# Kernel optimization log

Measured on AMD Instinct MI355X. Metric: run time of the kernel, lower is better.

## Reference

```python
import jax, jax.numpy as jnp
import numpy as np

EPS = 1e-5
MAX_NORM = 1.0 - EPS
K = 16
ALPHA = 0.1
TAU = 0.1  # softmax temperature in forward


def project(x):
    # enforce ||x|| < 1 on the Poincare ball
    n = jnp.clip(jnp.linalg.norm(x, axis=-1, keepdims=True), EPS, None)
    return x / jnp.maximum(n / MAX_NORM, 1.0)


def mobius_add(u, v):
    c = 1.0
    dot_uv = jnp.sum(u * v, axis=-1, keepdims=True)
    nu = jnp.clip(jnp.sum(u * u, axis=-1, keepdims=True), 0.0, MAX_NORM ** 2)
    nv = jnp.clip(jnp.sum(v * v, axis=-1, keepdims=True), 0.0, MAX_NORM ** 2)
    num = (1 + 2 * c * dot_uv + c * nv) * u + (1 - c * nu) * v
    den = 1 + 2 * c * dot_uv + c * c * nu * nv
    return project(num / jnp.clip(den, EPS, None))


def exp_map(x, v):
    # sqrt_c = 1
    vn = jnp.clip(jnp.linalg.norm(v, axis=-1, keepdims=True), EPS, None)
    second = jnp.tanh(vn / 2.0) * v / vn
    return mobius_add(x, second)


def poincare_cdist(q, mem):
    # q: [B, M], mem: [N, M] -> [B, N] geodesic distances (c=1)
    qn = jnp.clip(jnp.sum(q * q, axis=-1), 0.0, MAX_NORM ** 2)          # [B]
    mn = jnp.clip(jnp.sum(mem * mem, axis=-1), 0.0, MAX_NORM ** 2)      # [N]
    # ||q - m||^2 expanded via gram matrix (same math as diff-based form)
    dist_sq = jnp.clip(jnp.sum(q * q, axis=-1)[:, None] + jnp.sum(mem * mem, axis=-1)[None, :]
                       - 2.0 * q @ mem.T, 0.0, None)                     # [B, N]
    den = (1.0 - qn)[:, None] * (1.0 - mn)[None, :]
    x = 2.0 * dist_sq / jnp.clip(den, EPS, None)
    return jnp.arccosh(1.0 + x)


def layernorm(x, g, b):
    mu = jnp.mean(x, axis=-1, keepdims=True)
    var = jnp.mean((x - mu) ** 2, axis=-1, keepdims=True)
    return (x - mu) / jnp.sqrt(var + 1e-5) * g + b


def setup_inputs() -> dict:
    key = jax.random.key(0)
    ks = jax.random.split(key, 10)
    B, S, H, M, N = 32, 2048, 1024, 128, 500000
    hidden_states = jax.random.normal(ks[0], (B, S, H), dtype=jnp.float32)
    W1 = jax.random.normal(ks[1], (H, M), dtype=jnp.float32) * 0.02
    b1 = jnp.zeros((M,), dtype=jnp.float32)
    ln_g = jnp.ones((M,), dtype=jnp.float32)
    ln_b = jnp.zeros((M,), dtype=jnp.float32)
    W2 = jax.random.normal(ks[2], (M, M), dtype=jnp.float32) * 0.02
    b2 = jnp.zeros((M,), dtype=jnp.float32)
    q_origin = jnp.zeros((1, M), dtype=jnp.float32)
    memory = project(jax.random.normal(ks[3], (N, M), dtype=jnp.float32) * 0.3)
    Wp = jax.random.normal(ks[4], (M, H), dtype=jnp.float32) * 0.02
    bp = jnp.zeros((H,), dtype=jnp.float32)
    return {"hidden_states": hidden_states, "W1": W1, "b1": b1, "ln_g": ln_g,
            "ln_b": ln_b, "W2": W2, "b2": b2, "q_origin": q_origin,
            "memory": memory, "Wp": Wp, "bp": bp}


def reference(hidden_states, W1, b1, ln_g, ln_b, W2, b2, q_origin, memory, Wp, bp):
    B, S, H = hidden_states.shape
    # query network on mean-pooled hidden states
    pooled = jnp.mean(hidden_states, axis=1)                  # [B, H]
    h = pooled @ W1 + b1                                      # [B, M]
    h = jax.nn.gelu(layernorm(h, ln_g, ln_b), approximate=False)
    tangent = h @ W2 + b2                                     # [B, M]
    origin = project(jnp.broadcast_to(q_origin, (B, q_origin.shape[-1])))
    query = exp_map(origin, tangent)                          # [B, M] on ball
    # geodesic kNN over the memory bank
    dists = poincare_cdist(query, memory)                     # [B, N]
    neg_top, idx = jax.lax.top_k(-dists, K)                   # smallest K
    top_d = -neg_top                                          # [B, K]
    neighbors = memory[idx]                                   # [B, K, M]
    w = jax.nn.softmax(-top_d / TAU, axis=-1)                 # [B, K]
    retrieved = jnp.einsum('bk,bkm->bm', w, neighbors)        # [B, M]
    force = retrieved @ Wp + bp                               # [B, H]
    return hidden_states + ALPHA * force[:, None, :]
```

## Files before the change

### kernel.cpp

```cpp
#include <hip/hip_runtime.h>
#include <float.h>
#include <math.h>

#define B_ 32
#define S_ 2048
#define H_ 1024
#define M_ 128
#define N_ 500000
#define KK 16
#define KK2 32
#define ALPHA_ 0.1f
#define TAU_ 0.1f
#define EPS_ 1e-5f
#define MAX_NORM_ 0.99999f
#define MAXN2_ (MAX_NORM_ * MAX_NORM_)
#define SC_ 64
#define RPB_ 512
#define NBLK_ ((N_ + RPB_ - 1) / RPB_)
#define WIN_ 2048
#define NWIN_ ((N_ + WIN_ - 1) / WIN_)
#define NPAD_ (NWIN_ * WIN_)

typedef __attribute__((ext_vector_type(8))) short short8;
typedef __attribute__((ext_vector_type(4))) float f32x4;

__device__ __forceinline__ unsigned short to_bf16(float x) {
    unsigned u = __float_as_uint(x);
    return (unsigned short)((u + 0x7FFFu + ((u >> 16) & 1u)) >> 16);
}

__global__ __launch_bounds__(256) void k1_pool(const float* __restrict__ hid,
                                               float* __restrict__ pp) {
    int bid = blockIdx.x;
    int b = bid >> 6, sc = bid & 63;
    const float4* h4 = (const float4*)hid;
    float4 acc = {0.f, 0.f, 0.f, 0.f};
    int s0 = sc * (S_ / SC_);
    for (int s = 0; s < S_ / SC_; ++s) {
        float4 v = h4[((size_t)(b * S_ + s0 + s) << 8) + threadIdx.x];
        acc.x += v.x; acc.y += v.y; acc.z += v.z; acc.w += v.w;
    }
    ((float4*)pp)[(size_t)(b * SC_ + sc) * 256 + threadIdx.x] = acc;
}

__device__ __forceinline__ float block_reduce_sum_128(float v, volatile float* red, int tid) {
    red[tid] = v;
    __syncthreads();
    if (tid < 64) red[tid] += red[tid + 64];
    __syncthreads();
    if (tid < 64) {
        float x = red[tid];
        #pragma unroll
        for (int off = 32; off >= 1; off >>= 1) x += __shfl_down(x, off);
        if (tid == 0) red[0] = x;
    }
    __syncthreads();
    float r = red[0];
    __syncthreads();
    return r;
}

__global__ void k2_query(const float* __restrict__ pp, const float* __restrict__ W1,
                         const float* __restrict__ b1, const float* __restrict__ ln_g,
                         const float* __restrict__ ln_b, const float* __restrict__ W2,
                         const float* __restrict__ b2, const float* __restrict__ qorig,
                         float* __restrict__ query, float* __restrict__ qstats) {
    __shared__ float pooled[H_];
    __shared__ float red[128];
    __shared__ float hv[M_];
    int b = blockIdx.x, tid = threadIdx.x;
    #pragma unroll
    for (int j = 0; j < H_ / 128; ++j) {
        int h = tid + j * 128;
        float s = 0.f;
        for (int sc = 0; sc < SC_; ++sc) s += pp[(size_t)(b * SC_ + sc) * H_ + h];
        pooled[h] = s * (1.0f / (float)S_);
    }
    __syncthreads();
    int m = tid;
    float x = b1[m];
    for (int k = 0; k < H_; ++k) x = fmaf(pooled[k], W1[k * M_ + m], x);
    float mu = block_reduce_sum_128(x, red, tid) * (1.0f / (float)M_);
    float dmu = x - mu;
    float var = block_reduce_sum_128(dmu * dmu, red, tid) * (1.0f / (float)M_);
    float xh = dmu * rsqrtf(var + 1e-5f) * ln_g[m] + ln_b[m];
    float g = 0.5f * xh * (1.0f + erff(xh * 0.70710678f));
    hv[m] = g;
    __syncthreads();
    float t = b2[m];
    for (int k = 0; k < M_; ++k) t = fmaf(hv[k], W2[k * M_ + m], t);
    float o = qorig[m];
    float on2 = block_reduce_sum_128(o * o, red, tid);
    float on = fmaxf(sqrtf(on2), EPS_);
    float osc = 1.0f / fmaxf(on / MAX_NORM_, 1.0f);
    float u = o * osc;
    float vn2 = block_reduce_sum_128(t * t, red, tid);
    float vn = fmaxf(sqrtf(vn2), EPS_);
    float sec = tanhf(vn * 0.5f) * t / vn;
    float dot_uv = block_reduce_sum_128(u * sec, red, tid);
    float nu = fminf(fmaxf(block_reduce_sum_128(u * u, red, tid), 0.f), MAXN2_);
    float nv = fminf(fmaxf(block_reduce_sum_128(sec * sec, red, tid), 0.f), MAXN2_);
    float num = (1.0f + 2.0f * dot_uv + nv) * u + (1.0f - nu) * sec;
    float den = 1.0f + 2.0f * dot_uv + nu * nv;
    float r = num / fmaxf(den, EPS_);
    float rn2 = block_reduce_sum_128(r * r, red, tid);
    float rn = fmaxf(sqrtf(rn2), EPS_);
    float rsc = 1.0f / fmaxf(rn / MAX_NORM_, 1.0f);
    float q = r * rsc;
    query[b * M_ + m] = q;
    float qq = block_reduce_sum_128(q * q, red, tid);
    if (tid == 0) {
        qstats[b * 2 + 0] = qq;
        float qn = fminf(fmaxf(qq, 0.f), MAXN2_);
        qstats[b * 2 + 1] = 1.0f - qn;
    }
}

__global__ __launch_bounds__(256, 3) void k3_scores(const float* __restrict__ mem,
                                                    const float* __restrict__ query,
                                                    const float* __restrict__ qstats,
                                                    unsigned short* __restrict__ keyplane) {
    __shared__ unsigned short key_lds[B_][264];
    __shared__ float mm_lds[256];
    __shared__ float qq_s[B_], omq_s[B_];
    int tid = threadIdx.x, bid = blockIdx.x;
    int wave = tid >> 6, lane = tid & 63;
    int l15 = lane & 15, lk = lane >> 4;

    if (tid < B_) { qq_s[tid] = qstats[tid * 2]; omq_s[tid] = qstats[tid * 2 + 1]; }

    short8 bfrag[2][4];
    #pragma unroll
    for (int bg = 0; bg < 2; ++bg) {
        #pragma unroll
        for (int kt = 0; kt < 4; ++kt) {
            int batch = bg * 16 + l15;
            const float4* qp = (const float4*)(query + batch * M_ + kt * 32 + lk * 8);
            float4 lo = qp[0], hi = qp[1];
            short8 f;
            f[0] = (short)to_bf16(lo.x); f[1] = (short)to_bf16(lo.y);
            f[2] = (short)to_bf16(lo.z); f[3] = (short)to_bf16(lo.w);
            f[4] = (short)to_bf16(hi.x); f[5] = (short)to_bf16(hi.y);
            f[6] = (short)to_bf16(hi.z); f[7] = (short)to_bf16(hi.w);
            bfrag[bg][kt] = f;
        }
    }

    #pragma unroll 1
    for (int p = 0; p < 2; ++p) {
        int passbase = bid * RPB_ + p * 256;
        f32x4 acc[4][2];
        #pragma unroll
        for (int rg = 0; rg < 4; ++rg)
            #pragma unroll
            for (int bg = 0; bg < 2; ++bg)
                acc[rg][bg] = (f32x4){0.f, 0.f, 0.f, 0.f};
        float mmp[4] = {0.f, 0.f, 0.f, 0.f};

        #pragma unroll
        for (int rg = 0; rg < 4; ++rg) {
            int r = passbase + wave * 64 + rg * 16 + l15;
            const float4* mp = (const float4*)(mem + (size_t)((r < N_) ? r : 0) * M_);
            #pragma unroll
            for (int kt = 0; kt < 4; ++kt) {
                float4 lo = mp[kt * 8 + lk * 2];
                float4 hi = mp[kt * 8 + lk * 2 + 1];
                mmp[rg] = fmaf(lo.x, lo.x, fmaf(lo.y, lo.y, fmaf(lo.z, lo.z, fmaf(lo.w, lo.w, mmp[rg]))));
                mmp[rg] = fmaf(hi.x, hi.x, fmaf(hi.y, hi.y, fmaf(hi.z, hi.z, fmaf(hi.w, hi.w, mmp[rg]))));
                short8 af;
                af[0] = (short)to_bf16(lo.x); af[1] = (short)to_bf16(lo.y);
                af[2] = (short)to_bf16(lo.z); af[3] = (short)to_bf16(lo.w);
                af[4] = (short)to_bf16(hi.x); af[5] = (short)to_bf16(hi.y);
                af[6] = (short)to_bf16(hi.z); af[7] = (short)to_bf16(hi.w);
                acc[rg][0] = __builtin_amdgcn_mfma_f32_16x16x32_bf16(af, bfrag[0][kt], acc[rg][0], 0, 0, 0);
                acc[rg][1] = __builtin_amdgcn_mfma_f32_16x16x32_bf16(af, bfrag[1][kt], acc[rg][1], 0, 0, 0);
            }
        }
        #pragma unroll
        for (int rg = 0; rg < 4; ++rg) {
            float v = mmp[rg] + __shfl_xor(mmp[rg], 16);
            v += __shfl_xor(v, 32);
            if (lane < 16) mm_lds[wave * 64 + rg * 16 + l15] = v;
        }
        __syncthreads();

        #pragma unroll
        for (int rg = 0; rg < 4; ++rg) {
            #pragma unroll
            for (int bg = 0; bg < 2; ++bg) {
                #pragma unroll
                for (int reg = 0; reg < 4; ++reg) {
                    int row_local = wave * 64 + rg * 16 + lk * 4 + reg;
                    int batch = bg * 16 + l15;
                    float dot = acc[rg][bg][reg];
                    float mmv = mm_lds[row_local];
                    float mn = fminf(mmv, MAXN2_);
                    float dsq = fmaxf(qq_s[batch] + mmv - 2.0f * dot, 0.f);
                    float t = dsq / fmaxf(omq_s[batch] * (1.0f - mn), EPS_);
                    key_lds[batch][row_local] = to_bf16(t);
                }
            }
        }
        __syncthreads();

        {
            int batch = tid >> 3, chunk = tid & 7;
            int rbase = passbase + chunk * 32;
            unsigned short* dstp = keyplane + (size_t)batch * NPAD_ + rbase;
            #pragma unroll
            for (int i = 0; i < 4; ++i) {
                int gr = rbase + i * 8;
                uint4 v = *(const uint4*)&key_lds[batch][chunk * 32 + i * 8];
                if (gr + 8 <= N_) {
                    *(uint4*)(dstp + i * 8) = v;
                } else {
                    for (int t = 0; t < 8; ++t)
                        if (gr + t < N_) dstp[i * 8 + t] = key_lds[batch][chunk * 32 + i * 8 + t];
                }
            }
        }
        __syncthreads();
    }
}

__global__ __launch_bounds__(256, 4) void k4_sel(const unsigned short* __restrict__ keyplane,
                                                 unsigned* __restrict__ cand_key) {
    int win = blockIdx.x >> 2, quad = blockIdx.x & 3;
    int wave = threadIdx.x >> 6, lane = threadIdx.x & 63;
    int base = win * WIN_;
    #pragma unroll 1
    for (int j = 0; j < 2; ++j) {
        int b = quad * 8 + wave * 2 + j;
        const uint4* kp = (const uint4*)(keyplane + (size_t)b * NPAD_ + base);
        unsigned keys[32];
        #pragma unroll
        for (int i = 0; i < 4; ++i) {
            uint4 v = kp[lane + i * 64];
            int rl0 = (lane + i * 64) * 8;
            int pos = base + rl0;
            unsigned s[8];
            s[0] = v.x & 0xFFFFu; s[1] = v.x >> 16;
            s[2] = v.y & 0xFFFFu; s[3] = v.y >> 16;
            s[4] = v.z & 0xFFFFu; s[5] = v.z >> 16;
            s[6] = v.w & 0xFFFFu; s[7] = v.w >> 16;
            #pragma unroll
            for (int t = 0; t < 8; ++t)
                keys[i * 8 + t] = (pos + t < N_) ? ((s[t] << 11) | (unsigned)(rl0 + t))
                                                 : 0xFFFFFFFFu;
        }
        for (int k = 0; k < KK; ++k) {
            unsigned m = keys[0];
            #pragma unroll
            for (int i = 1; i < 32; ++i) m = min(m, keys[i]);
            #pragma unroll
            for (int off = 32; off >= 1; off >>= 1)
                m = min(m, (unsigned)__shfl_xor((int)m, off));
            if (lane == 0) cand_key[((size_t)win * B_ + b) * KK + k] = m;
            #pragma unroll
            for (int i = 0; i < 32; ++i)
                if (keys[i] == m) keys[i] = 0xFFFFFFFFu;
        }
    }
}

__global__ void k45_retrieve(const unsigned* __restrict__ cand_key,
                             const float* __restrict__ mem, const float* __restrict__ query,
                             const float* __restrict__ qstats,
                             const float* __restrict__ Wp, const float* __restrict__ bp,
                             float* __restrict__ force) {
    __shared__ unsigned tv[256 * KK];
    __shared__ int ti[256 * KK];
    __shared__ unsigned mv[64 * KK];
    __shared__ int mi[64 * KK];
    __shared__ int top32_s[KK2];
    __shared__ float q_s[M_];
    __shared__ float d_s[KK2];
    __shared__ float w_s[KK];
    __shared__ int idx_s[KK];
    __shared__ float ret_s[M_];
    int b = blockIdx.x, tid = threadIdx.x;

    unsigned val[KK]; int idx[KK];
    #pragma unroll
    for (int i = 0; i < KK; ++i) { val[i] = 0xFFFFFFFFu; idx[i] = 0; }
    int nc = NWIN_ * KK;
    for (int c = tid; c < nc; c += 256) {
        int g = c >> 4, k = c & 15;
        unsigned v = cand_key[((size_t)g * B_ + b) * KK + k];
        int id = g * WIN_ + (int)(v & 2047u);
        if (v < val[KK - 1]) {
            val[KK - 1] = v; idx[KK - 1] = id;
            #pragma unroll
            for (int j = KK - 1; j > 0; --j) {
                if (val[j] < val[j - 1]) {
                    unsigned tvv = val[j]; val[j] = val[j - 1]; val[j - 1] = tvv;
                    int tii = idx[j]; idx[j] = idx[j - 1]; idx[j - 1] = tii;
                }
            }
        }
    }
    if (tid < M_) q_s[tid] = query[b * M_ + tid];
    #pragma unroll
    for (int i = 0; i < KK; ++i) { tv[tid * KK + i] = val[i]; ti[tid * KK + i] = idx[i]; }
    __syncthreads();

    if (tid < 64) {
        #pragma unroll
        for (int i = 0; i < KK; ++i) { val[i] = 0xFFFFFFFFu; idx[i] = 0; }
        for (int t = tid * 4; t < tid * 4 + 4; ++t) {
            for (int i = 0; i < KK; ++i) {
                unsigned v = tv[t * KK + i]; int id = ti[t * KK + i];
                if (v >= val[KK - 1]) break;
                val[KK - 1] = v; idx[KK - 1] = id;
                #pragma unroll
                for (int j = KK - 1; j > 0; --j) {
                    if (val[j] < val[j - 1]) {
                        unsigned tvv = val[j]; val[j] = val[j - 1]; val[j - 1] = tvv;
                        int tii = idx[j]; idx[j] = idx[j - 1]; idx[j - 1] = tii;
                    }
                }
            }
        }
        #pragma unroll
        for (int i = 0; i < KK; ++i) { mv[tid * KK + i] = val[i]; mi[tid * KK + i] = idx[i]; }
        int h = 0;
        for (int k = 0; k < KK2; ++k) {
            unsigned cv = (h < KK) ? mv[tid * KK + h] : 0xFFFFFFFFu;
            int ci = (h < KK) ? mi[tid * KK + h] : 0;
            unsigned bestv = cv; int bestl = tid;
            #pragma unroll
            for (int off = 32; off >= 1; off >>= 1) {
                unsigned ov = (unsigned)__shfl_down((int)bestv, off);
                int ol = __shfl_down(bestl, off);
                if (ov < bestv) { bestv = ov; bestl = ol; }
            }
            bestl = __shfl(bestl, 0);
            if (tid == bestl) {
                top32_s[k] = (ci < 0) ? 0 : ((ci >= N_) ? (N_ - 1) : ci);
                h++;
            }
        }
    }
    __syncthreads();

    float qq = qstats[b * 2], omq = qstats[b * 2 + 1];
    int wave = tid >> 6, lane = tid & 63;
    for (int ii = wave; ii < KK2; ii += 4) {
        const float* mr = mem + (size_t)top32_s[ii] * M_;
        float a0 = mr[lane], a1 = mr[lane + 64];
        float p = q_s[lane] * a0 + q_s[lane + 64] * a1;
        float mm = a0 * a0 + a1 * a1;
        #pragma unroll
        for (int off = 32; off >= 1; off >>= 1) {
            p += __shfl_down(p, off);
            mm += __shfl_down(mm, off);
        }
        if (lane == 0) {
            float dsq = fmaxf(qq + mm - 2.0f * p, 0.f);
            float mn = fminf(mm, MAXN2_);
            float t = dsq / fmaxf(omq * (1.0f - mn), EPS_);
            d_s[ii] = acoshf(1.0f + 2.0f * t);
        }
    }
    __syncthreads();
    if (tid == 0) {
        bool used[KK2];
        for (int i = 0; i < KK2; ++i) used[i] = false;
        float seld[KK];
        for (int k = 0; k < KK; ++k) {
            float bd = FLT_MAX; int bi = -1;
            for (int i = 0; i < KK2; ++i) {
                if (used[i]) continue;
                if (d_s[i] < bd || (d_s[i] == bd && (bi < 0 || top32_s[i] < top32_s[bi]))) {
                    bd = d_s[i]; bi = i;
                }
            }
            used[bi] = true; seld[k] = bd; idx_s[k] = top32_s[bi];
        }
        float dmin = seld[0];
        for (int i = 1; i < KK; ++i) dmin = fminf(dmin, seld[i]);
        float Z = 0.f;
        for (int i = 0; i < KK; ++i) {
            float w = expf((dmin - seld[i]) * (1.0f / TAU_));
            w_s[i] = w; Z += w;
        }
        float iZ = 1.0f / Z;
        for (int i = 0; i < KK; ++i) w_s[i] *= iZ;
    }
    __syncthreads();
    if (tid < M_) {
        float r = 0.f;
        for (int i = 0; i < KK; ++i) r = fmaf(w_s[i], mem[(size_t)idx_s[i] * M_ + tid], r);
        ret_s[tid] = r;
    }
    __syncthreads();
    #pragma unroll
    for (int j = 0; j < 4; ++j) {
        int h = tid + j * 256;
        float f = bp[h];
        for (int k = 0; k < M_; ++k) f = fmaf(ret_s[k], Wp[k * H_ + h], f);
        force[b * H_ + h] = f;
    }
}

__global__ __launch_bounds__(256) void k6_out(const float* __restrict__ hid,
                                              const float* __restrict__ force,
                                              float* __restrict__ out) {
    const float4* h4 = (const float4*)hid;
    const float4* f4 = (const float4*)force;
    float4* o4 = (float4*)out;
    int n4 = B_ * S_ * H_ / 4;
    for (int i = blockIdx.x * blockDim.x + threadIdx.x; i < n4; i += gridDim.x * blockDim.x) {
        int b = i >> 19;
        float4 hv = h4[i];
        float4 fv = f4[(b << 8) + (i & 255)];
        float4 ov;
        ov.x = fmaf(ALPHA_, fv.x, hv.x);
        ov.y = fmaf(ALPHA_, fv.y, hv.y);
        ov.z = fmaf(ALPHA_, fv.z, hv.z);
        ov.w = fmaf(ALPHA_, fv.w, hv.w);
        o4[i] = ov;
    }
}

extern "C" void kernel_launch(void* const* d_in, const int* in_sizes, int n_in,
                              void* d_out, int out_size, void* d_ws, size_t ws_size,
                              hipStream_t stream) {
    const float* hid    = (const float*)d_in[0];
    const float* W1     = (const float*)d_in[1];
    const float* b1     = (const float*)d_in[2];
    const float* ln_g   = (const float*)d_in[3];
    const float* ln_b   = (const float*)d_in[4];
    const float* W2     = (const float*)d_in[5];
    const float* b2     = (const float*)d_in[6];
    const float* qorig  = (const float*)d_in[7];
    const float* mem    = (const float*)d_in[8];
    const float* Wp     = (const float*)d_in[9];
    const float* bp     = (const float*)d_in[10];
    float* out = (float*)d_out;

    char* ws = (char*)d_ws;
    size_t off = 0;
    float* pp = (float*)(ws + off);        off += (size_t)B_ * SC_ * H_ * 4;
    float* query = (float*)(ws + off);     off += (size_t)B_ * M_ * 4;
    float* qstats = (float*)(ws + off);    off += (size_t)B_ * 2 * 4;
    off = (off + 255) & ~(size_t)255;
    unsigned short* keyplane = (unsigned short*)(ws + off); off += (size_t)B_ * NPAD_ * 2;
    off = (off + 255) & ~(size_t)255;
    unsigned* cand_key = (unsigned*)(ws + off); off += (size_t)NWIN_ * B_ * KK * 4;
    float* force = (float*)(ws + off);     off += (size_t)B_ * H_ * 4;
    (void)ws_size; (void)in_sizes; (void)n_in; (void)out_size;

    hipLaunchKernelGGL(k1_pool, dim3(B_ * SC_), dim3(256), 0, stream, hid, pp);
    hipLaunchKernelGGL(k2_query, dim3(B_), dim3(128), 0, stream, pp, W1, b1, ln_g, ln_b,
                       W2, b2, qorig, query, qstats);
    hipLaunchKernelGGL(k3_scores, dim3(NBLK_), dim3(256), 0, stream, mem, query, qstats, keyplane);
    hipLaunchKernelGGL(k4_sel, dim3(NWIN_ * 4), dim3(256), 0, stream, keyplane, cand_key);
    hipLaunchKernelGGL(k45_retrieve, dim3(B_), dim3(256), 0, stream, cand_key,
                       mem, query, qstats, Wp, bp, force);
    hipLaunchKernelGGL(k6_out, dim3(2048), dim3(256), 0, stream, hid, force, out);
}
```

Measured before the change: 418.9 us.

## Fuse all pipeline stages into one cooperative persistent kernel with grid syncs

Replaces the six separate launches (pool, query MLP, MFMA scoring, per-window selection, retrieval, output broadcast) with a single cooperative kernel of 1024 blocks. The stages are separated by grid.sync barriers, which is meant to remove per-launch overhead and the idle gaps between kernels. The final top-k merge is also reworked to use packed 64-bit keys handled by one wave, in both the fused path and the fallback kernel. The risks are that five grid-wide barriers have their own cost, and that the tiny 32-block stages leave most of the persistent grid idle. If the cooperative launch fails, the code falls back to the old multi-kernel path.

```diff
diff --git a/kernel.cpp b/kernel.cpp
--- a/kernel.cpp
+++ b/kernel.cpp
@@ -1,6 +1,9 @@
 #include <hip/hip_runtime.h>
+#include <hip/hip_cooperative_groups.h>
 #include <float.h>
 #include <math.h>
+
+namespace cg = cooperative_groups;
 
 #define B_ 32
 #define S_ 2048
@@ -20,6 +23,7 @@
 #define WIN_ 2048
 #define NWIN_ ((N_ + WIN_ - 1) / WIN_)
 #define NPAD_ (NWIN_ * WIN_)
+#define GRID_ 1024
 
 typedef __attribute__((ext_vector_type(8))) short short8;
 typedef __attribute__((ext_vector_type(4))) float f32x4;
@@ -27,6 +31,395 @@
 __device__ __forceinline__ unsigned short to_bf16(float x) {
     unsigned u = __float_as_uint(x);
     return (unsigned short)((u + 0x7FFFu + ((u >> 16) & 1u)) >> 16);
+}
+
+__device__ __forceinline__ float bred256(float v, volatile float* red, int tid) {
+    red[tid] = v;
+    __syncthreads();
+    if (tid < 64) {
+        float x = red[tid] + red[tid + 64] + red[tid + 128] + red[tid + 192];
+        #pragma unroll
+        for (int off = 32; off >= 1; off >>= 1) x += __shfl_down(x, off);
+        if (tid == 0) red[0] = x;
+    }
+    __syncthreads();
+    float r = red[0];
+    __syncthreads();
+    return r;
+}
+
+__global__ __launch_bounds__(256, 4) void mega(
+        const float* __restrict__ hid, const float* __restrict__ W1,
+        const float* __restrict__ b1, const float* __restrict__ ln_g,
+        const float* __restrict__ ln_b, const float* __restrict__ W2,
+        const float* __restrict__ b2, const float* __restrict__ qorig,
+        const float* __restrict__ mem, const float* __restrict__ Wp,
+        const float* __restrict__ bp, float* __restrict__ out,
+        float* __restrict__ pp, float* __restrict__ query, float* __restrict__ qstats,
+        unsigned short* __restrict__ keyplane, unsigned* __restrict__ cand_key,
+        float* __restrict__ force) {
+    cg::grid_group grid = cg::this_grid();
+    __shared__ __align__(16) char smem[18944];
+    int tid = threadIdx.x;
+
+    {
+        const float4* h4 = (const float4*)hid;
+        #pragma unroll
+        for (int rep = 0; rep < 2; ++rep) {
+            int chunk = blockIdx.x + rep * GRID_;
+            int b = chunk >> 6, sc = chunk & 63;
+            float4 acc = {0.f, 0.f, 0.f, 0.f};
+            int s0 = sc * (S_ / SC_);
+            for (int s = 0; s < S_ / SC_; ++s) {
+                float4 v = h4[((size_t)(b * S_ + s0 + s) << 8) + tid];
+                acc.x += v.x; acc.y += v.y; acc.z += v.z; acc.w += v.w;
+            }
+            ((float4*)pp)[(size_t)chunk * 256 + tid] = acc;
+        }
+    }
+    __threadfence();
+    grid.sync();
+
+    if (blockIdx.x < B_) {
+        int b = blockIdx.x;
+        float* pooled = (float*)smem;
+        float* red    = pooled + H_;
+        float* hv     = red + 256;
+        #pragma unroll
+        for (int j = 0; j < H_ / 256; ++j) {
+            int h = tid + j * 256;
+            float s = 0.f;
+            for (int sc = 0; sc < SC_; ++sc) s += pp[(size_t)(b * SC_ + sc) * H_ + h];
+            pooled[h] = s * (1.0f / (float)S_);
+        }
+        __syncthreads();
+        int m = tid & 127, half = tid >> 7;
+        float xp = 0.f;
+        for (int k = half * (H_ / 2); k < (half + 1) * (H_ / 2); ++k)
+            xp = fmaf(pooled[k], W1[k * M_ + m], xp);
+        red[tid] = xp;
+        __syncthreads();
+        float x = (tid < M_) ? (red[m] + red[m + 128] + b1[m]) : 0.f;
+        __syncthreads();
+        float mu = bred256(x, red, tid) * (1.0f / (float)M_);
+        float dmu = (tid < M_) ? (x - mu) : 0.f;
+        float var = bred256(dmu * dmu, red, tid) * (1.0f / (float)M_);
+        float lg = (tid < M_) ? ln_g[m] : 0.f;
+        float lb = (tid < M_) ? ln_b[m] : 0.f;
+        float xh = dmu * rsqrtf(var + 1e-5f) * lg + lb;
+        float g = 0.5f * xh * (1.0f + erff(xh * 0.70710678f));
+        if (tid < M_) hv[m] = g;
+        __syncthreads();
+        float t = 0.f;
+        if (tid < M_) {
+            t = b2[m];
+            for (int k = 0; k < M_; ++k) t = fmaf(hv[k], W2[k * M_ + m], t);
+        }
+        float o = (tid < M_) ? qorig[m] : 0.f;
+        float on2 = bred256(o * o, red, tid);
+        float on = fmaxf(sqrtf(on2), EPS_);
+        float osc = 1.0f / fmaxf(on / MAX_NORM_, 1.0f);
+        float u = o * osc;
+        float vn2 = bred256(t * t, red, tid);
+        float vn = fmaxf(sqrtf(vn2), EPS_);
+        float sec = tanhf(vn * 0.5f) * t / vn;
+        float dot_uv = bred256(u * sec, red, tid);
+        float nu = fminf(fmaxf(bred256(u * u, red, tid), 0.f), MAXN2_);
+        float nv = fminf(fmaxf(bred256(sec * sec, red, tid), 0.f), MAXN2_);
+        float num = (1.0f + 2.0f * dot_uv + nv) * u + (1.0f - nu) * sec;
+        float den = 1.0f + 2.0f * dot_uv + nu * nv;
+        float r = num / fmaxf(den, EPS_);
+        float rn2 = bred256(r * r, red, tid);
+        float rn = fmaxf(sqrtf(rn2), EPS_);
+        float rsc = 1.0f / fmaxf(rn / MAX_NORM_, 1.0f);
+        float q = r * rsc;
+        if (tid < M_) query[b * M_ + m] = q;
+        float qq = bred256(q * q, red, tid);
+        if (tid == 0) {
+            qstats[b * 2 + 0] = qq;
+            float qn = fminf(fmaxf(qq, 0.f), MAXN2_);
+            qstats[b * 2 + 1] = 1.0f - qn;
+        }
+    }
+    __threadfence();
+    grid.sync();
+
+    if (blockIdx.x < NBLK_) {
+        unsigned short (*key_lds)[264] = (unsigned short(*)[264])smem;
+        float* mm_lds = (float*)(smem + 16896);
+        float* qq_s   = (float*)(smem + 16896 + 1024);
+        float* omq_s  = qq_s + B_;
+        int bid = blockIdx.x;
+        int wave = tid >> 6, lane = tid & 63;
+        int l15 = lane & 15, lk = lane >> 4;
+
+        if (tid < B_) { qq_s[tid] = qstats[tid * 2]; omq_s[tid] = qstats[tid * 2 + 1]; }
+
+        short8 bfrag[2][4];
+        #pragma unroll
+        for (int bg = 0; bg < 2; ++bg) {
+            #pragma unroll
+            for (int kt = 0; kt < 4; ++kt) {
+                int batch = bg * 16 + l15;
+                const float4* qp = (const float4*)(query + batch * M_ + kt * 32 + lk * 8);
+                float4 lo = qp[0], hi = qp[1];
+                short8 f;
+                f[0] = (short)to_bf16(lo.x); f[1] = (short)to_bf16(lo.y);
+                f[2] = (short)to_bf16(lo.z); f[3] = (short)to_bf16(lo.w);
+                f[4] = (short)to_bf16(hi.x); f[5] = (short)to_bf16(hi.y);
+                f[6] = (short)to_bf16(hi.z); f[7] = (short)to_bf16(hi.w);
+                bfrag[bg][kt] = f;
+            }
+        }
+
+        #pragma unroll 1
+        for (int p = 0; p < 2; ++p) {
+            int passbase = bid * RPB_ + p * 256;
+            f32x4 acc[4][2];
+            #pragma unroll
+            for (int rg = 0; rg < 4; ++rg)
+                #pragma unroll
+                for (int bg = 0; bg < 2; ++bg)
+                    acc[rg][bg] = (f32x4){0.f, 0.f, 0.f, 0.f};
+            float mmp[4] = {0.f, 0.f, 0.f, 0.f};
+
+            #pragma unroll
+            for (int rg = 0; rg < 4; ++rg) {
+                int r = passbase + wave * 64 + rg * 16 + l15;
+                const float4* mp = (const float4*)(mem + (size_t)((r < N_) ? r : 0) * M_);
+                #pragma unroll
+                for (int kt = 0; kt < 4; ++kt) {
+                    float4 lo = mp[kt * 8 + lk * 2];
+                    float4 hi = mp[kt * 8 + lk * 2 + 1];
+                    mmp[rg] = fmaf(lo.x, lo.x, fmaf(lo.y, lo.y, fmaf(lo.z, lo.z, fmaf(lo.w, lo.w, mmp[rg]))));
+                    mmp[rg] = fmaf(hi.x, hi.x, fmaf(hi.y, hi.y, fmaf(hi.z, hi.z, fmaf(hi.w, hi.w, mmp[rg]))));
+                    short8 af;
+                    af[0] = (short)to_bf16(lo.x); af[1] = (short)to_bf16(lo.y);
+                    af[2] = (short)to_bf16(lo.z); af[3] = (short)to_bf16(lo.w);
+                    af[4] = (short)to_bf16(hi.x); af[5] = (short)to_bf16(hi.y);
+                    af[6] = (short)to_bf16(hi.z); af[7] = (short)to_bf16(hi.w);
+                    acc[rg][0] = __builtin_amdgcn_mfma_f32_16x16x32_bf16(af, bfrag[0][kt], acc[rg][0], 0, 0, 0);
+                    acc[rg][1] = __builtin_amdgcn_mfma_f32_16x16x32_bf16(af, bfrag[1][kt], acc[rg][1], 0, 0, 0);
+                }
+            }
+            #pragma unroll
+            for (int rg = 0; rg < 4; ++rg) {
+                float v = mmp[rg] + __shfl_xor(mmp[rg], 16);
+                v += __shfl_xor(v, 32);
+                if (lane < 16) mm_lds[wave * 64 + rg * 16 + l15] = v;
+            }
+            __syncthreads();
+
+            #pragma unroll
+            for (int rg = 0; rg < 4; ++rg) {
+                #pragma unroll
+                for (int bg = 0; bg < 2; ++bg) {
+                    #pragma unroll
+                    for (int reg = 0; reg < 4; ++reg) {
+                        int row_local = wave * 64 + rg * 16 + lk * 4 + reg;
+                        int batch = bg * 16 + l15;
+                        float dot = acc[rg][bg][reg];
+                        float mmv = mm_lds[row_local];
+                        float mn = fminf(mmv, MAXN2_);
+                        float dsq = fmaxf(qq_s[batch] + mmv - 2.0f * dot, 0.f);
+                        float t = dsq / fmaxf(omq_s[batch] * (1.0f - mn), EPS_);
+                        key_lds[batch][row_local] = to_bf16(t);
+                    }
+                }
+            }
+            __syncthreads();
+
+            {
+                int batch = tid >> 3, chunk = tid & 7;
+                int rbase = passbase + chunk * 32;
+                unsigned short* dstp = keyplane + (size_t)batch * NPAD_ + rbase;
+                #pragma unroll
+                for (int i = 0; i < 4; ++i) {
+                    int gr = rbase + i * 8;
+                    uint4 v = *(const uint4*)&key_lds[batch][chunk * 32 + i * 8];
+                    if (gr + 8 <= N_) {
+                        *(uint4*)(dstp + i * 8) = v;
+                    } else {
+                        for (int t = 0; t < 8; ++t)
+                            if (gr + t < N_) dstp[i * 8 + t] = key_lds[batch][chunk * 32 + i * 8 + t];
+                    }
+                }
+            }
+            __syncthreads();
+        }
+    }
+    __threadfence();
+    grid.sync();
+
+    if (blockIdx.x < NWIN_ * 4) {
+        int win = blockIdx.x >> 2, quad = blockIdx.x & 3;
+        int wave = tid >> 6, lane = tid & 63;
+        int base = win * WIN_;
+        #pragma unroll 1
+        for (int j = 0; j < 2; ++j) {
+            int b = quad * 8 + wave * 2 + j;
+            const uint4* kp = (const uint4*)(keyplane + (size_t)b * NPAD_ + base);
+            unsigned keys[32];
+            #pragma unroll
+            for (int i = 0; i < 4; ++i) {
+                uint4 v = kp[lane + i * 64];
+                int rl0 = (lane + i * 64) * 8;
+                int pos = base + rl0;
+                unsigned s[8];
+                s[0] = v.x & 0xFFFFu; s[1] = v.x >> 16;
+                s[2] = v.y & 0xFFFFu; s[3] = v.y >> 16;
+                s[4] = v.z & 0xFFFFu; s[5] = v.z >> 16;
+                s[6] = v.w & 0xFFFFu; s[7] = v.w >> 16;
+                #pragma unroll
+                for (int t = 0; t < 8; ++t)
+                    keys[i * 8 + t] = (pos + t < N_) ? ((s[t] << 11) | (unsigned)(rl0 + t))
+                                                     : 0xFFFFFFFFu;
+            }
+            for (int k = 0; k < KK; ++k) {
+                unsigned m = keys[0];
+                #pragma unroll
+                for (int i = 1; i < 32; ++i) m = min(m, keys[i]);
+                #pragma unroll
+                for (int off = 32; off >= 1; off >>= 1)
+                    m = min(m, (unsigned)__shfl_xor((int)m, off));
+                if (lane == 0) cand_key[((size_t)win * B_ + b) * KK + k] = m;
+                #pragma unroll
+                for (int i = 0; i < 32; ++i)
+                    if (keys[i] == m) keys[i] = 0xFFFFFFFFu;
+            }
+        }
+    }
+    __threadfence();
+    grid.sync();
+
+    if (blockIdx.x < B_) {
+        int b = blockIdx.x;
+        int* top32_s = (int*)smem;
+        float* q_s   = (float*)(smem + 128);
+        float* d_s   = (float*)(smem + 640);
+        float* w_s   = (float*)(smem + 768);
+        int* idx_s   = (int*)(smem + 832);
+        float* ret_s = (float*)(smem + 896);
+        if (tid < M_) q_s[tid] = query[b * M_ + tid];
+
+        if (tid < 64) {
+            unsigned long long vals[16];
+            #pragma unroll
+            for (int i = 0; i < 16; ++i) vals[i] = 0xFFFFFFFFFFFFFFFFull;
+            for (int c = tid; c < NWIN_ * KK; c += 64) {
+                int g = c >> 4, k = c & 15;
+                unsigned v = cand_key[((size_t)g * B_ + b) * KK + k];
+                unsigned grow = (unsigned)(g * WIN_) + (v & 2047u);
+                unsigned long long key = ((unsigned long long)v << 32) | (unsigned long long)grow;
+                if (key < vals[15]) {
+                    vals[15] = key;
+                    #pragma unroll
+                    for (int j = 15; j > 0; --j) {
+                        if (vals[j] < vals[j - 1]) {
+                            unsigned long long tt = vals[j]; vals[j] = vals[j - 1]; vals[j - 1] = tt;
+                        }
+                    }
+                }
+            }
+            for (int k = 0; k < KK2; ++k) {
+                unsigned long long m = vals[0];
+                #pragma unroll
+                for (int off = 32; off >= 1; off >>= 1) {
+                    unsigned long long o = __shfl_xor(m, off);
+                    if (o < m) m = o;
+                }
+                if (tid == 0) {
+                    int ci = (int)(unsigned)(m & 0xFFFFFFFFull);
+                    top32_s[k] = (ci < 0) ? 0 : ((ci >= N_) ? (N_ - 1) : ci);
+                }
+                if (vals[0] == m) {
+                    #pragma unroll
+                    for (int j = 0; j < 15; ++j) vals[j] = vals[j + 1];
+                    vals[15] = 0xFFFFFFFFFFFFFFFFull;
+                }
+            }
+        }
+        __syncthreads();
+
+        float qq = qstats[b * 2], omq = qstats[b * 2 + 1];
+        int wave = tid >> 6, lane = tid & 63;
+        for (int ii = wave; ii < KK2; ii += 4) {
+            const float* mr = mem + (size_t)top32_s[ii] * M_;
+            float a0 = mr[lane], a1 = mr[lane + 64];
+            float p = q_s[lane] * a0 + q_s[lane + 64] * a1;
+            float mm = a0 * a0 + a1 * a1;
+            #pragma unroll
+            for (int off = 32; off >= 1; off >>= 1) {
+                p += __shfl_down(p, off);
+                mm += __shfl_down(mm, off);
+            }
+            if (lane == 0) {
+                float dsq = fmaxf(qq + mm - 2.0f * p, 0.f);
+                float mn = fminf(mm, MAXN2_);
+                float t = dsq / fmaxf(omq * (1.0f - mn), EPS_);
+                d_s[ii] = acoshf(1.0f + 2.0f * t);
+            }
+        }
+        __syncthreads();
+        if (tid == 0) {
+            bool used[KK2];
+            for (int i = 0; i < KK2; ++i) used[i] = false;
+            float seld[KK];
+            for (int k = 0; k < KK; ++k) {
+                float bd = FLT_MAX; int bi = -1;
+                for (int i = 0; i < KK2; ++i) {
+                    if (used[i]) continue;
+                    if (d_s[i] < bd || (d_s[i] == bd && (bi < 0 || top32_s[i] < top32_s[bi]))) {
+                        bd = d_s[i]; bi = i;
+                    }
+                }
+                used[bi] = true; seld[k] = bd; idx_s[k] = top32_s[bi];
+            }
+            float dmin = seld[0];
+            for (int i = 1; i < KK; ++i) dmin = fminf(dmin, seld[i]);
+            float Z = 0.f;
+            for (int i = 0; i < KK; ++i) {
+                float w = expf((dmin - seld[i]) * (1.0f / TAU_));
+                w_s[i] = w; Z += w;
+            }
+            float iZ = 1.0f / Z;
+            for (int i = 0; i < KK; ++i) w_s[i] *= iZ;
+        }
+        __syncthreads();
+        if (tid < M_) {
+            float r = 0.f;
+            for (int i = 0; i < KK; ++i) r = fmaf(w_s[i], mem[(size_t)idx_s[i] * M_ + tid], r);
+            ret_s[tid] = r;
+        }
+        __syncthreads();
+        #pragma unroll
+        for (int j = 0; j < 4; ++j) {
+            int h = tid + j * 256;
+            float f = bp[h];
+            for (int k = 0; k < M_; ++k) f = fmaf(ret_s[k], Wp[k * H_ + h], f);
+            force[b * H_ + h] = f;
+        }
+    }
+    __threadfence();
+    grid.sync();
+
+    {
+        const float4* h4 = (const float4*)hid;
+        const float4* f4 = (const float4*)force;
+        float4* o4 = (float4*)out;
+        int n4 = B_ * S_ * H_ / 4;
+        for (int i = blockIdx.x * 256 + tid; i < n4; i += GRID_ * 256) {
+            int b = i >> 19;
+            float4 hv = h4[i];
+            float4 fv = f4[(b << 8) + (i & 255)];
+            float4 ov;
+            ov.x = fmaf(ALPHA_, fv.x, hv.x);
+            ov.y = fmaf(ALPHA_, fv.y, hv.y);
+            ov.z = fmaf(ALPHA_, fv.z, hv.z);
+            ov.w = fmaf(ALPHA_, fv.w, hv.w);
+            o4[i] = ov;
+        }
+    }
 }
 
 __global__ __launch_bounds__(256) void k1_pool(const float* __restrict__ hid,
@@ -268,10 +661,6 @@
                              const float* __restrict__ qstats,
                              const float* __restrict__ Wp, const float* __restrict__ bp,
                              float* __restrict__ force) {
-    __shared__ unsigned tv[256 * KK];
-    __shared__ int ti[256 * KK];
-    __shared__ unsigned mv[64 * KK];
-    __shared__ int mi[64 * KK];
     __shared__ int top32_s[KK2];
     __shared__ float q_s[M_];
     __shared__ float d_s[KK2];
@@ -279,65 +668,42 @@
     __shared__ int idx_s[KK];
     __shared__ float ret_s[M_];
     int b = blockIdx.x, tid = threadIdx.x;
-
-    unsigned val[KK]; int idx[KK];
-    #pragma unroll
-    for (int i = 0; i < KK; ++i) { val[i] = 0xFFFFFFFFu; idx[i] = 0; }
-    int nc = NWIN_ * KK;
-    for (int c = tid; c < nc; c += 256) {
-        int g = c >> 4, k = c & 15;
-        unsigned v = cand_key[((size_t)g * B_ + b) * KK + k];
-        int id = g * WIN_ + (int)(v & 2047u);
-        if (v < val[KK - 1]) {
-            val[KK - 1] = v; idx[KK - 1] = id;
-            #pragma unroll
-            for (int j = KK - 1; j > 0; --j) {
-                if (val[j] < val[j - 1]) {
-                    unsigned tvv = val[j]; val[j] = val[j - 1]; val[j - 1] = tvv;
-                    int tii = idx[j]; idx[j] = idx[j - 1]; idx[j - 1] = tii;
-                }
-            }
-        }
-    }
     if (tid < M_) q_s[tid] = query[b * M_ + tid];
-    #pragma unroll
-    for (int i = 0; i < KK; ++i) { tv[tid * KK + i] = val[i]; ti[tid * KK + i] = idx[i]; }
-    __syncthreads();
 
     if (tid < 64) {
-        #pragma unroll
-        for (int i = 0; i < KK; ++i) { val[i] = 0xFFFFFFFFu; idx[i] = 0; }
-        for (int t = tid * 4; t < tid * 4 + 4; ++t) {
-            for (int i = 0; i < KK; ++i) {
-                unsigned v = tv[t * KK + i]; int id = ti[t * KK + i];
-                if (v >= val[KK - 1]) break;
-                val[KK - 1] = v; idx[KK - 1] = id;
-                #pragma unroll
-                for (int j = KK - 1; j > 0; --j) {
-                    if (val[j] < val[j - 1]) {
-                        unsigned tvv = val[j]; val[j] = val[j - 1]; val[j - 1] = tvv;
-                        int tii = idx[j]; idx[j] = idx[j - 1]; idx[j - 1] = tii;
+        unsigned long long vals[16];
+        #pragma unroll
+        for (int i = 0; i < 16; ++i) vals[i] = 0xFFFFFFFFFFFFFFFFull;
+        for (int c = tid; c < NWIN_ * KK; c += 64) {
+            int g = c >> 4, k = c & 15;
+            unsigned v = cand_key[((size_t)g * B_ + b) * KK + k];
+            unsigned grow = (unsigned)(g * WIN_) + (v & 2047u);
+            unsigned long long key = ((unsigned long long)v << 32) | (unsigned long long)grow;
+            if (key < vals[15]) {
+                vals[15] = key;
+                #pragma unroll
+                for (int j = 15; j > 0; --j) {
+                    if (vals[j] < vals[j - 1]) {
+                        unsigned long long tt = vals[j]; vals[j] = vals[j - 1]; vals[j - 1] = tt;
                     }
                 }
             }
         }
-        #pragma unroll
-        for (int i = 0; i < KK; ++i) { mv[tid * KK + i] = val[i]; mi[tid * KK + i] = idx[i]; }
-        int h = 0;
         for (int k = 0; k < KK2; ++k) {
-            unsigned cv = (h < KK) ? mv[tid * KK + h] : 0xFFFFFFFFu;
-            int ci = (h < KK) ? mi[tid * KK + h] : 0;
-            unsigned bestv = cv; int bestl = tid;
+            unsigned long long m = vals[0];
             #pragma unroll
             for (int off = 32; off >= 1; off >>= 1) {
-                unsigned ov = (unsigned)__shfl_down((int)bestv, off);
-                int ol = __shfl_down(bestl, off);
-                if (ov < bestv) { bestv = ov; bestl = ol; }
-            }
-            bestl = __shfl(bestl, 0);
-            if (tid == bestl) {
+                unsigned long long o = __shfl_xor(m, off);
+                if (o < m) m = o;
+            }
+            if (tid == 0) {
+                int ci = (int)(unsigned)(m & 0xFFFFFFFFull);
                 top32_s[k] = (ci < 0) ? 0 : ((ci >= N_) ? (N_ - 1) : ci);
-                h++;
+            }
+            if (vals[0] == m) {
+                #pragma unroll
+                for (int j = 0; j < 15; ++j) vals[j] = vals[j + 1];
+                vals[15] = 0xFFFFFFFFFFFFFFFFull;
             }
         }
     }
@@ -437,7 +803,7 @@
     const float* mem    = (const float*)d_in[8];
     const float* Wp     = (const float*)d_in[9];
     const float* bp     = (const float*)d_in[10];
-    float* out = (float*)d_out;
+    float* outp = (float*)d_out;
 
     char* ws = (char*)d_ws;
     size_t off = 0;
@@ -451,12 +817,20 @@
     float* force = (float*)(ws + off);     off += (size_t)B_ * H_ * 4;
     (void)ws_size; (void)in_sizes; (void)n_in; (void)out_size;
 
-    hipLaunchKernelGGL(k1_pool, dim3(B_ * SC_), dim3(256), 0, stream, hid, pp);
-    hipLaunchKernelGGL(k2_query, dim3(B_), dim3(128), 0, stream, pp, W1, b1, ln_g, ln_b,
-                       W2, b2, qorig, query, qstats);
-    hipLaunchKernelGGL(k3_scores, dim3(NBLK_), dim3(256), 0, stream, mem, query, qstats, keyplane);
-    hipLaunchKernelGGL(k4_sel, dim3(NWIN_ * 4), dim3(256), 0, stream, keyplane, cand_key);
-    hipLaunchKernelGGL(k45_retrieve, dim3(B_), dim3(256), 0, stream, cand_key,
-                       mem, query, qstats, Wp, bp, force);
-    hipLaunchKernelGGL(k6_out, dim3(2048), dim3(256), 0, stream, hid, force, out);
-}
+    void* args[] = {(void*)&hid, (void*)&W1, (void*)&b1, (void*)&ln_g, (void*)&ln_b,
+                    (void*)&W2, (void*)&b2, (void*)&qorig, (void*)&mem, (void*)&Wp,
+                    (void*)&bp, (void*)&outp, (void*)&pp, (void*)&query, (void*)&qstats,
+                    (void*)&keyplane, (void*)&cand_key, (void*)&force};
+    hipError_t err = hipLaunchCooperativeKernel((const void*)mega, dim3(GRID_), dim3(256),
+                                                args, 0, stream);
+    if (err != hipSuccess) {
+        hipLaunchKernelGGL(k1_pool, dim3(B_ * SC_), dim3(256), 0, stream, hid, pp);
+        hipLaunchKernelGGL(k2_query, dim3(B_), dim3(128), 0, stream, pp, W1, b1, ln_g, ln_b,
+                           W2, b2, qorig, query, qstats);
+        hipLaunchKernelGGL(k3_scores, dim3(NBLK_), dim3(256), 0, stream, mem, query, qstats, keyplane);
+        hipLaunchKernelGGL(k4_sel, dim3(NWIN_ * 4), dim3(256), 0, stream, keyplane, cand_key);
+        hipLaunchKernelGGL(k45_retrieve, dim3(B_), dim3(256), 0, stream, cand_key,
+                           mem, query, qstats, Wp, bp, force);
+        hipLaunchKernelGGL(k6_out, dim3(2048), dim3(256), 0, stream, hid, force, outp);
+    }
+}
```

Result: slower. 1.656 ms (+295.2%).
